# Kernel tuning notes

Measured on AMD Instinct MI355X. Metric: run time of the kernel, lower is better.

The kernel has to match this reference:

```python
import jax, jax.numpy as jnp
import numpy as np
import math

B, LQ, LK = 4, 1024, 2048
QD, KD, VD = 768, 512, 512
H, NH = 1024, 16
HD = H // NH

def setup_inputs() -> dict:
    key = jax.random.key(0)
    ks = jax.random.split(key, 11)
    s = 0.02
    return {
        "query": jax.random.normal(ks[0], (B, LQ, QD), jnp.float32),
        "key": jax.random.normal(ks[1], (B, LK, KD), jnp.float32),
        "value": jax.random.normal(ks[2], (B, LK, VD), jnp.float32),
        "Wq": jax.random.normal(ks[3], (QD, H), jnp.float32) * s,
        "bq": jnp.zeros((H,), jnp.float32),
        "Wk": jax.random.normal(ks[4], (KD, H), jnp.float32) * s,
        "bk": jnp.zeros((H,), jnp.float32),
        "Wv": jax.random.normal(ks[5], (VD, H), jnp.float32) * s,
        "bv": jnp.zeros((H,), jnp.float32),
        "Wo": jax.random.normal(ks[6], (H, H), jnp.float32) * s,
        "bo": jnp.zeros((H,), jnp.float32),
    }

def reference(query, key, value, Wq, bq, Wk, bk, Wv, bv, Wo, bo):
    # project and split heads: [B, L, H] -> [B, NH, L, HD]
    def heads(x):
        b, l, _ = x.shape
        return x.reshape(b, l, NH, HD).transpose(0, 2, 1, 3)
    q = heads(query @ Wq + bq)   # [B, NH, LQ, HD]
    k = heads(key @ Wk + bk)     # [B, NH, LK, HD]
    v = heads(value @ Wv + bv)   # [B, NH, LK, HD]
    scores = jnp.einsum('bhqd,bhkd->bhqk', q, k) / math.sqrt(HD)
    weights = jax.nn.softmax(scores, axis=-1)  # dropout inactive (eval / rate used deterministically as identity)
    att = jnp.einsum('bhqk,bhkd->bhqd', weights, v)
    att = att.transpose(0, 2, 1, 3).reshape(query.shape[0], -1, H)
    out = att @ Wo + bo
    return out
```

## Files before the change

kernel.cpp:

```cpp
#include <hip/hip_runtime.h>
#include <math.h>

using bf16x8 = __attribute__((ext_vector_type(8))) short;
using f32x4  = __attribute__((ext_vector_type(4))) float;
using u32x2  = __attribute__((ext_vector_type(2))) unsigned int;

namespace {
constexpr int kB  = 4;
constexpr int kLQ = 1024;
constexpr int kLK = 2048;
constexpr int kH  = 1024;
constexpr int kHD = 64;
}

__device__ __forceinline__ unsigned short f2bf(float x) {
  union { float f; unsigned int u; } v; v.f = x;
  unsigned int r = v.u + 0x7fffu + ((v.u >> 16) & 1u);
  return (unsigned short)(r >> 16);
}

typedef const __attribute__((address_space(1))) unsigned int guint_t;
typedef __attribute__((address_space(3))) unsigned int luint_t;
__device__ __forceinline__ void g2l16(const void* g, void* l) {
  __builtin_amdgcn_global_load_lds(
      (guint_t*)g,
      (luint_t*)(unsigned int)(unsigned long long)l,
      16, 0, 0);
}

__global__ __launch_bounds__(256) void prep_kernel(
    const float* __restrict__ q, const float* __restrict__ k,
    const float* __restrict__ v, const float* __restrict__ Wq,
    const float* __restrict__ Wk, const float* __restrict__ Wv,
    const float* __restrict__ Wo, unsigned short* __restrict__ qo,
    unsigned short* __restrict__ ko, unsigned short* __restrict__ vo,
    unsigned short* __restrict__ WqT, unsigned short* __restrict__ WkT,
    unsigned short* __restrict__ WvT, unsigned short* __restrict__ WoT)
{
  __shared__ float tile[64][65];
  const int t = threadIdx.x;
  if (blockIdx.x < 5632) {
    int c = blockIdx.x * 256 + t;
    const float* src; unsigned short* dst;
    if (c < 393216)      { src = q; dst = qo; }
    else if (c < 917504) { src = k; dst = ko; c -= 393216; }
    else                 { src = v; dst = vo; c -= 917504; }
    const int i = c * 8;
    const float4 a = *(const float4*)(src + i);
    const float4 b = *(const float4*)(src + i + 4);
    uint4 o;
    o.x = (unsigned int)f2bf(a.x) | ((unsigned int)f2bf(a.y) << 16);
    o.y = (unsigned int)f2bf(a.z) | ((unsigned int)f2bf(a.w) << 16);
    o.z = (unsigned int)f2bf(b.x) | ((unsigned int)f2bf(b.y) << 16);
    o.w = (unsigned int)f2bf(b.z) | ((unsigned int)f2bf(b.w) << 16);
    *(uint4*)(dst + i) = o;
    return;
  }
  int id = blockIdx.x - 5632;
  const float* W; unsigned short* Wt; int Kd;
  if (id < 192)      { W = Wq; Wt = WqT; Kd = 768; }
  else if (id < 320) { W = Wk; Wt = WkT; Kd = 512;  id -= 192; }
  else if (id < 448) { W = Wv; Wt = WvT; Kd = 512;  id -= 320; }
  else               { W = Wo; Wt = WoT; Kd = 1024; id -= 448; }
  const int Nd = 1024;
  const int n0 = (id & 15) * 64;
  const int k0 = (id >> 4) * 64;
  const int rr = t >> 4;
  const int c4 = t & 15;
#pragma unroll
  for (int i = 0; i < 4; ++i) {
    const int row = i * 16 + rr;
    const float4 vv = *(const float4*)(W + (size_t)(k0 + row) * Nd + n0 + c4 * 4);
    tile[row][c4*4+0] = vv.x; tile[row][c4*4+1] = vv.y;
    tile[row][c4*4+2] = vv.z; tile[row][c4*4+3] = vv.w;
  }
  __syncthreads();
#pragma unroll
  for (int i = 0; i < 4; ++i) {
    const int n = i * 16 + rr;
    ushort4 o;
    o.x = f2bf(tile[c4*4+0][n]); o.y = f2bf(tile[c4*4+1][n]);
    o.z = f2bf(tile[c4*4+2][n]); o.w = f2bf(tile[c4*4+3][n]);
    *(ushort4*)(Wt + (size_t)(n0 + n) * Kd + k0 + c4 * 4) = o;
  }
}

__device__ __forceinline__ void gemm_body(
    const unsigned short* __restrict__ A, const unsigned short* __restrict__ Bt,
    const float* __restrict__ bias, void* __restrict__ Cout,
    int N, int K, int bx, int by, int mode, float scale, char* lds)
{
  const int t    = threadIdx.x;
  const int lane = t & 63;
  const int w    = t >> 6;
  const int l15  = lane & 15;
  const int lq8  = (lane >> 4) * 8;
  const int lq4  = (lane >> 4) * 4;
  const int r0   = by * 128;
  const int c0   = bx * 128;
  const int wm   = w >> 1, wn = w & 1;

  f32x4 acc[4][4] = {};

  const unsigned short* gsrc[4];
  char* ldst[4];
#pragma unroll
  for (int i = 0; i < 4; ++i) {
    const int g = w * 4 + i;
    const unsigned short* src = (g < 8) ? A : Bt;
    const int rbase = (g < 8) ? (r0 + g * 16) : (c0 + (g - 8) * 16);
    gsrc[i] = src + (size_t)(rbase + l15) * K + lq8;
    ldst[i] = lds + g * 1024 + lane * 16;
  }

#pragma unroll
  for (int i = 0; i < 4; ++i) g2l16(gsrc[i], ldst[i]);
#pragma unroll
  for (int i = 0; i < 4; ++i) g2l16(gsrc[i] + 32, ldst[i] + 16384);

  int slot = 0;
  for (int k0 = 0; k0 < K; k0 += 32) {
    if (k0 + 32 < K) {
      asm volatile("s_waitcnt vmcnt(4)\n\ts_barrier" ::: "memory");
    } else {
      asm volatile("s_waitcnt vmcnt(0)\n\ts_barrier" ::: "memory");
    }
    char* buf = lds + slot * 16384;
    if (k0 + 64 < K) {
      int ns = slot + 2; if (ns >= 3) ns -= 3;
      char* noff = ldst[0] - (lds + 0) + (char*)0; (void)noff;
#pragma unroll
      for (int i = 0; i < 4; ++i)
        g2l16(gsrc[i] + k0 + 64, ldst[i] + ns * 16384);
    }
    bf16x8 af[4], bfr[4];
#pragma unroll
    for (int i = 0; i < 4; ++i) af[i]  = *(const bf16x8*)(buf + (wm*4 + i) * 1024 + lane * 16);
#pragma unroll
    for (int j = 0; j < 4; ++j) bfr[j] = *(const bf16x8*)(buf + 8192 + (wn*4 + j) * 1024 + lane * 16);
#pragma unroll
    for (int i = 0; i < 4; ++i)
#pragma unroll
      for (int j = 0; j < 4; ++j)
        acc[i][j] = __builtin_amdgcn_mfma_f32_16x16x32_bf16(af[i], bfr[j], acc[i][j], 0, 0, 0);
    slot = (slot == 2) ? 0 : slot + 1;
  }

#pragma unroll
  for (int j = 0; j < 4; ++j) {
    const int col = c0 + wn * 64 + j * 16 + l15;
    const float bcol = bias[col];
#pragma unroll
    for (int i = 0; i < 4; ++i) {
      const int row = r0 + wm * 64 + i * 16 + lq4;
      if (mode == 0) {
        float* out = (float*)Cout;
#pragma unroll
        for (int r = 0; r < 4; ++r) out[(size_t)(row + r) * N + col] = acc[i][j][r] + bcol;
      } else if (mode == 1) {
        unsigned short* out = (unsigned short*)Cout;
#pragma unroll
        for (int r = 0; r < 4; ++r) out[(size_t)(row + r) * N + col] = f2bf((acc[i][j][r] + bcol) * scale);
      } else {
        unsigned short* out = (unsigned short*)Cout;
        const int bb = row >> 11;
        const int lk = row & 2047;
        ushort4 o;
        o.x = f2bf(acc[i][j][0] + bcol); o.y = f2bf(acc[i][j][1] + bcol);
        o.z = f2bf(acc[i][j][2] + bcol); o.w = f2bf(acc[i][j][3] + bcol);
        *(ushort4*)(out + (size_t)(bb * kH + col) * kLK + lk) = o;
      }
    }
  }
}

__global__ __launch_bounds__(256) void qkv_gemm_kernel(
    const unsigned short* __restrict__ qA, const unsigned short* __restrict__ WqT,
    const float* __restrict__ bq, unsigned short* __restrict__ Qb,
    const unsigned short* __restrict__ kA, const unsigned short* __restrict__ WkT,
    const float* __restrict__ bk, unsigned short* __restrict__ Kb,
    const unsigned short* __restrict__ vA, const unsigned short* __restrict__ WvT,
    const float* __restrict__ bv, unsigned short* __restrict__ Vtw)
{
  __shared__ __align__(16) char lds[49152];
  int id = blockIdx.x;
  if (id < 256) {
    gemm_body(qA, WqT, bq, Qb, 1024, 768, id & 7, id >> 3, 1,
              0.18033688011112042f, lds);
  } else if (id < 768) {
    id -= 256;
    gemm_body(kA, WkT, bk, Kb, 1024, 512, id & 7, id >> 3, 1, 1.f, lds);
  } else {
    id -= 768;
    gemm_body(vA, WvT, bv, Vtw, 1024, 512, id & 7, id >> 3, 2, 1.f, lds);
  }
}

__global__ __launch_bounds__(256) void out_gemm_kernel(
    const unsigned short* __restrict__ A, const unsigned short* __restrict__ Bt,
    const float* __restrict__ bias, float* __restrict__ C)
{
  __shared__ __align__(16) char lds[49152];
  const int id = blockIdx.x;
  gemm_body(A, Bt, bias, C, 1024, 1024, id & 7, id >> 3, 0, 1.f, lds);
}

__global__ __launch_bounds__(256) void attn_mfma_kernel(
    const unsigned short* __restrict__ Q, const unsigned short* __restrict__ K,
    const unsigned short* __restrict__ Vt, unsigned short* __restrict__ O)
{
  __shared__ __align__(16) char lds[51200];
  constexpr int POFF = 32768;
  const int t    = threadIdx.x;
  const int lane = t & 63;
  const int w    = t >> 6;
  const int l15  = lane & 15;
  const int lg   = lane >> 4;
  const int lq8  = lg * 8;
  const int lq4  = lg * 4;
  const int flat = blockIdx.x;
  const int bh   = flat & 63;
  const int qb   = flat >> 6;
  const int h    = bh & 15;
  const int b    = bh >> 4;
  const int q0   = qb * 128;
  const int hoff = h * kHD;

  bf16x8 qf[2][2];
#pragma unroll
  for (int qi = 0; qi < 2; ++qi)
#pragma unroll
    for (int kh = 0; kh < 2; ++kh)
      qf[qi][kh] = *(const bf16x8*)(Q + (size_t)(b*kLQ + q0 + w*32 + qi*16 + l15) * kH
                                      + hoff + kh*32 + lq8);

  f32x4 acc[2][4] = {};
  float lsum[2] = {0.f, 0.f};

  char* const pwr = lds + POFF + (w*32 + l15) * 144 + lq4 * 2;
  const char* const prd = lds + POFF + (w*32 + l15) * 144 + lq8 * 2;

#pragma unroll
  for (int i = 0; i < 4; ++i) {
    const int g = w * 4 + i;
    if (g < 8) {
      g2l16(K + (size_t)(b*kLK + (g >> 1)*16 + l15) * kH + hoff + (g & 1)*32 + lq8,
            lds + g * 1024 + lane * 16);
    } else {
      const int gg = g - 8;
      g2l16(Vt + (size_t)(b*kH + hoff + (gg >> 1)*16 + l15) * kLK + (gg & 1)*32 + lq8,
            lds + 8192 + gg * 1024 + lane * 16);
    }
  }

  int pb = 0;
  for (int kt = 0; kt < kLK / 64; ++kt, pb ^= 1) {
    __syncthreads();
    char* buf = lds + pb * 16384;
    if (kt + 1 < kLK / 64) {
      char* nbuf = lds + (pb ^ 1) * 16384;
      const int kc1 = (kt + 1) * 64;
#pragma unroll
      for (int i = 0; i < 4; ++i) {
        const int g = w * 4 + i;
        if (g < 8) {
          g2l16(K + (size_t)(b*kLK + kc1 + (g >> 1)*16 + l15) * kH + hoff + (g & 1)*32 + lq8,
                nbuf + g * 1024 + lane * 16);
        } else {
          const int gg = g - 8;
          g2l16(Vt + (size_t)(b*kH + hoff + (gg >> 1)*16 + l15) * kLK + kc1 + (gg & 1)*32 + lq8,
                nbuf + 8192 + gg * 1024 + lane * 16);
        }
      }
    }

    f32x4 s[2][4];
#pragma unroll
    for (int kcf = 0; kcf < 4; ++kcf) {
      const bf16x8 kf0 = *(const bf16x8*)(buf + (kcf*2 + 0) * 1024 + lane * 16);
      const bf16x8 kf1 = *(const bf16x8*)(buf + (kcf*2 + 1) * 1024 + lane * 16);
#pragma unroll
      for (int qi = 0; qi < 2; ++qi) {
        f32x4 z = {};
        z = __builtin_amdgcn_mfma_f32_16x16x32_bf16(kf0, qf[qi][0], z, 0, 0, 0);
        z = __builtin_amdgcn_mfma_f32_16x16x32_bf16(kf1, qf[qi][1], z, 0, 0, 0);
        s[qi][kcf] = z;
      }
    }

#pragma unroll
    for (int qi = 0; qi < 2; ++qi)
#pragma unroll
      for (int kcf = 0; kcf < 4; ++kcf) {
        const float p0 = __builtin_amdgcn_exp2f(s[qi][kcf][0]);
        const float p1 = __builtin_amdgcn_exp2f(s[qi][kcf][1]);
        const float p2 = __builtin_amdgcn_exp2f(s[qi][kcf][2]);
        const float p3 = __builtin_amdgcn_exp2f(s[qi][kcf][3]);
        lsum[qi] += (p0 + p1) + (p2 + p3);
        u32x2 pw;
        pw.x = __builtin_amdgcn_perm(__float_as_uint(p1), __float_as_uint(p0), 0x07060302u);
        pw.y = __builtin_amdgcn_perm(__float_as_uint(p3), __float_as_uint(p2), 0x07060302u);
        *(u32x2*)(pwr + qi*2304 + kcf*32) = pw;
      }

    bf16x8 pf[2][2];
#pragma unroll
    for (int qi = 0; qi < 2; ++qi)
#pragma unroll
      for (int kq = 0; kq < 2; ++kq)
        pf[qi][kq] = *(const bf16x8*)(prd + qi*2304 + kq*64);
#pragma unroll
    for (int vd = 0; vd < 4; ++vd) {
      const bf16x8 vf0 = *(const bf16x8*)(buf + 8192 + (vd*2 + 0) * 1024 + lane * 16);
      const bf16x8 vf1 = *(const bf16x8*)(buf + 8192 + (vd*2 + 1) * 1024 + lane * 16);
#pragma unroll
      for (int qi = 0; qi < 2; ++qi) {
        acc[qi][vd] = __builtin_amdgcn_mfma_f32_16x16x32_bf16(pf[qi][0], vf0, acc[qi][vd], 0, 0, 0);
        acc[qi][vd] = __builtin_amdgcn_mfma_f32_16x16x32_bf16(pf[qi][1], vf1, acc[qi][vd], 0, 0, 0);
      }
    }
  }

  float rinv[2][4];
#pragma unroll
  for (int qi = 0; qi < 2; ++qi) {
    float v = lsum[qi];
    v += __shfl_xor(v, 16);
    v += __shfl_xor(v, 32);
    v = 1.f / v;
#pragma unroll
    for (int r = 0; r < 4; ++r) rinv[qi][r] = __shfl(v, lq4 + r);
  }
#pragma unroll
  for (int qi = 0; qi < 2; ++qi)
#pragma unroll
    for (int vd = 0; vd < 4; ++vd)
#pragma unroll
      for (int r = 0; r < 4; ++r)
        O[(size_t)(b*kLQ + q0 + w*32 + qi*16 + lq4 + r) * kH + hoff + vd*16 + l15] =
            f2bf(acc[qi][vd][r] * rinv[qi][r]);
}

extern "C" void kernel_launch(void* const* d_in, const int* in_sizes, int n_in,
                              void* d_out, int out_size, void* d_ws, size_t ws_size,
                              hipStream_t stream) {
  (void)in_sizes; (void)n_in; (void)out_size; (void)ws_size;
  const float* query = (const float*)d_in[0];
  const float* key   = (const float*)d_in[1];
  const float* value = (const float*)d_in[2];
  const float* Wq = (const float*)d_in[3];
  const float* bq = (const float*)d_in[4];
  const float* Wk = (const float*)d_in[5];
  const float* bk = (const float*)d_in[6];
  const float* Wv = (const float*)d_in[7];
  const float* bv = (const float*)d_in[8];
  const float* Wo = (const float*)d_in[9];
  const float* bo = (const float*)d_in[10];
  float* out = (float*)d_out;

  unsigned short* ws  = (unsigned short*)d_ws;
  unsigned short* qA  = ws;
  unsigned short* kA  = qA  + 3145728;
  unsigned short* vA  = kA  + 4194304;
  unsigned short* WqT = vA  + 4194304;
  unsigned short* WkT = WqT + 786432;
  unsigned short* WvT = WkT + 524288;
  unsigned short* WoT = WvT + 524288;
  unsigned short* Qb  = WoT + 1048576;
  unsigned short* Kb  = Qb  + 4194304;
  unsigned short* Vtw = Kb  + 8388608;
  unsigned short* Ab  = Vtw + 8388608;

  prep_kernel<<<6336, 256, 0, stream>>>(query, key, value, Wq, Wk, Wv, Wo,
                                        qA, kA, vA, WqT, WkT, WvT, WoT);
  qkv_gemm_kernel<<<1280, 256, 0, stream>>>(qA, WqT, bq, Qb,
                                            kA, WkT, bk, Kb,
                                            vA, WvT, bv, Vtw);
  attn_mfma_kernel<<<512, 256, 0, stream>>>(Qb, Kb, Vtw, Ab);
  out_gemm_kernel<<<256, 256, 0, stream>>>(Ab, WoT, bo, out);
}
```

Before: 231.6 us.

## Triple-buffer K/V loads in attention and swizzle the P tile in LDS

```diff
diff --git a/kernel.cpp b/kernel.cpp
--- a/kernel.cpp
+++ b/kernel.cpp
@@ -128,7 +128,6 @@
     char* buf = lds + slot * 16384;
     if (k0 + 64 < K) {
       int ns = slot + 2; if (ns >= 3) ns -= 3;
-      char* noff = ldst[0] - (lds + 0) + (char*)0; (void)noff;
 #pragma unroll
       for (int i = 0; i < 4; ++i)
         g2l16(gsrc[i] + k0 + 64, ldst[i] + ns * 16384);
@@ -209,8 +208,8 @@
     const unsigned short* __restrict__ Q, const unsigned short* __restrict__ K,
     const unsigned short* __restrict__ Vt, unsigned short* __restrict__ O)
 {
-  __shared__ __align__(16) char lds[51200];
-  constexpr int POFF = 32768;
+  __shared__ __align__(16) char lds[65536];
+  constexpr int POFF = 49152;
   const int t    = threadIdx.x;
   const int lane = t & 63;
   const int w    = t >> 6;
@@ -225,6 +224,7 @@
   const int b    = bh >> 4;
   const int q0   = qb * 128;
   const int hoff = h * kHD;
+  constexpr int NT = kLK / 64;
 
   bf16x8 qf[2][2];
 #pragma unroll
@@ -237,41 +237,45 @@
   f32x4 acc[2][4] = {};
   float lsum[2] = {0.f, 0.f};
 
-  char* const pwr = lds + POFF + (w*32 + l15) * 144 + lq4 * 2;
-  const char* const prd = lds + POFF + (w*32 + l15) * 144 + lq8 * 2;
-
+  const int swz  = ((l15 * 5) & 7) << 4;
+  const int colw = (lg * 8)  ^ swz;
+  const int colr = (lg * 16) ^ swz;
+
+  const unsigned short* gsrc[4];
+  int gstep[4];
+  char* ldst[4];
 #pragma unroll
   for (int i = 0; i < 4; ++i) {
     const int g = w * 4 + i;
     if (g < 8) {
-      g2l16(K + (size_t)(b*kLK + (g >> 1)*16 + l15) * kH + hoff + (g & 1)*32 + lq8,
-            lds + g * 1024 + lane * 16);
+      gsrc[i]  = K + (size_t)(b*kLK + (g >> 1)*16 + l15) * kH + hoff + (g & 1)*32 + lq8;
+      gstep[i] = 64 * kH;
     } else {
       const int gg = g - 8;
-      g2l16(Vt + (size_t)(b*kH + hoff + (gg >> 1)*16 + l15) * kLK + (gg & 1)*32 + lq8,
-            lds + 8192 + gg * 1024 + lane * 16);
-    }
-  }
-
-  int pb = 0;
-  for (int kt = 0; kt < kLK / 64; ++kt, pb ^= 1) {
-    __syncthreads();
-    char* buf = lds + pb * 16384;
-    if (kt + 1 < kLK / 64) {
-      char* nbuf = lds + (pb ^ 1) * 16384;
-      const int kc1 = (kt + 1) * 64;
-#pragma unroll
-      for (int i = 0; i < 4; ++i) {
-        const int g = w * 4 + i;
-        if (g < 8) {
-          g2l16(K + (size_t)(b*kLK + kc1 + (g >> 1)*16 + l15) * kH + hoff + (g & 1)*32 + lq8,
-                nbuf + g * 1024 + lane * 16);
-        } else {
-          const int gg = g - 8;
-          g2l16(Vt + (size_t)(b*kH + hoff + (gg >> 1)*16 + l15) * kLK + kc1 + (gg & 1)*32 + lq8,
-                nbuf + 8192 + gg * 1024 + lane * 16);
-        }
-      }
+      gsrc[i]  = Vt + (size_t)(b*kH + hoff + (gg >> 1)*16 + l15) * kLK + (gg & 1)*32 + lq8;
+      gstep[i] = 64;
+    }
+    ldst[i] = lds + g * 1024 + lane * 16;
+  }
+
+#pragma unroll
+  for (int i = 0; i < 4; ++i) g2l16(gsrc[i], ldst[i]);
+#pragma unroll
+  for (int i = 0; i < 4; ++i) g2l16(gsrc[i] + gstep[i], ldst[i] + 16384);
+
+  int slot = 0;
+  for (int kt = 0; kt < NT; ++kt) {
+    if (kt + 1 < NT) {
+      asm volatile("s_waitcnt vmcnt(4)\n\ts_barrier" ::: "memory");
+    } else {
+      asm volatile("s_waitcnt vmcnt(0)\n\ts_barrier" ::: "memory");
+    }
+    char* buf = lds + slot * 16384;
+    if (kt + 2 < NT) {
+      int ns = slot + 2; if (ns >= 3) ns -= 3;
+#pragma unroll
+      for (int i = 0; i < 4; ++i)
+        g2l16(gsrc[i] + (size_t)(kt + 2) * gstep[i], ldst[i] + ns * 16384);
     }
 
     f32x4 s[2][4];
@@ -289,7 +293,8 @@
     }
 
 #pragma unroll
-    for (int qi = 0; qi < 2; ++qi)
+    for (int qi = 0; qi < 2; ++qi) {
+      char* const prow = lds + POFF + (w*32 + qi*16 + l15) * 128;
 #pragma unroll
       for (int kcf = 0; kcf < 4; ++kcf) {
         const float p0 = __builtin_amdgcn_exp2f(s[qi][kcf][0]);
@@ -300,15 +305,18 @@
         u32x2 pw;
         pw.x = __builtin_amdgcn_perm(__float_as_uint(p1), __float_as_uint(p0), 0x07060302u);
         pw.y = __builtin_amdgcn_perm(__float_as_uint(p3), __float_as_uint(p2), 0x07060302u);
-        *(u32x2*)(pwr + qi*2304 + kcf*32) = pw;
+        *(u32x2*)(prow + (colw ^ (kcf * 32))) = pw;
       }
+    }
 
     bf16x8 pf[2][2];
 #pragma unroll
-    for (int qi = 0; qi < 2; ++qi)
+    for (int qi = 0; qi < 2; ++qi) {
+      const char* const prow = lds + POFF + (w*32 + qi*16 + l15) * 128;
 #pragma unroll
       for (int kq = 0; kq < 2; ++kq)
-        pf[qi][kq] = *(const bf16x8*)(prd + qi*2304 + kq*64);
+        pf[qi][kq] = *(const bf16x8*)(prow + (colr ^ (kq * 64)));
+    }
 #pragma unroll
     for (int vd = 0; vd < 4; ++vd) {
       const bf16x8 vf0 = *(const bf16x8*)(buf + 8192 + (vd*2 + 0) * 1024 + lane * 16);
@@ -319,6 +327,7 @@
         acc[qi][vd] = __builtin_amdgcn_mfma_f32_16x16x32_bf16(pf[qi][1], vf1, acc[qi][vd], 0, 0, 0);
       }
     }
+    slot = (slot == 2) ? 0 : slot + 1;
   }
 
   float rinv[2][4];
```

Result: no change. 230.2 us (-0.6%).
